# Kernel optimization log

Measured on AMD Instinct MI355X. Metric: run time of the kernel, lower is better.

## Reference

```python
import jax, jax.numpy as jnp
import numpy as np

D_WIN = 6
SIGMA = D_WIN / 2.0  # sigma = D/2
EPS = 1e-6


def _ln(x, g, b):
    m = jnp.mean(x, -1, keepdims=True)
    v = jnp.var(x, -1, keepdims=True)
    return (x - m) / jnp.sqrt(v + EPS) * g + b


def _cross_attn(q, kv, Wq, Wkv, Wproj, bproj, nh):
    # standard multi-head cross attention, no qkv bias (qkv_bias=False)
    B, S, C = q.shape
    N = kv.shape[1]
    hd = C // nh
    scale = hd ** -0.5
    qh = (q @ Wq).reshape(B, S, nh, hd).transpose(0, 2, 1, 3) * scale
    kvh = (kv @ Wkv).reshape(B, N, 2, nh, hd).transpose(2, 0, 3, 1, 4)
    k, v = kvh[0], kvh[1]
    attn = jax.nn.softmax(jnp.einsum('bhsd,bhnd->bhsn', qh, k), -1)
    x = jnp.einsum('bhsn,bhnd->bhsd', attn, v).transpose(0, 2, 1, 3).reshape(B, S, C)
    return x @ Wproj + bproj


def setup_inputs() -> dict:
    key = jax.random.key(0)
    ks = jax.random.split(key, 32)
    B, S, C, H, W = 32, 128, 384, 8, 512

    def lin(k, i, o):
        return jax.random.normal(k, (i, o), jnp.float32) * 0.02

    inp = {
        'q': jax.random.normal(ks[0], (B, S, C), jnp.float32),
        'kv': jax.random.normal(ks[1], (B, H * W, C), jnp.float32),
        # main attention linears (qkv_bias=False)
        'Wq': lin(ks[2], C, C),
        'Wkv': lin(ks[3], C, 2 * C),
        'Wproj': lin(ks[4], C, C), 'bproj': jnp.zeros((C,), jnp.float32),
        # position predictor
        'Wp_w': lin(ks[5], C, C), 'Wp_b': jnp.zeros((C,), jnp.float32),
        'vp_w': lin(ks[6], C, 1), 'vp_b': jnp.zeros((1,), jnp.float32),
        'Wqpos': lin(ks[7], C, C), 'bqpos': jnp.zeros((C,), jnp.float32),
        # simplified RCTC decoder projection
        'Wrctc': lin(ks[8], C, C), 'brctc': jnp.zeros((C,), jnp.float32),
        # pt_to_question cross attention (2 heads)
        'ca1_Wq': lin(ks[9], C, C), 'ca1_Wkv': lin(ks[10], C, 2 * C),
        'ca1_Wproj': lin(ks[11], C, C), 'ca1_bproj': jnp.zeros((C,), jnp.float32),
        # pt_to_image cross attention (2 heads)
        'ca2_Wq': lin(ks[12], C, C), 'ca2_Wkv': lin(ks[13], C, 2 * C),
        'ca2_Wproj': lin(ks[14], C, C), 'ca2_bproj': jnp.zeros((C,), jnp.float32),
        # layernorms
        'g_q1': jnp.ones((C,), jnp.float32), 'b_q1': jnp.zeros((C,), jnp.float32),
        'g_kv1': jnp.ones((C,), jnp.float32), 'b_kv1': jnp.zeros((C,), jnp.float32),
        'g_q2': jnp.ones((C,), jnp.float32), 'b_q2': jnp.zeros((C,), jnp.float32),
        'g_kv2': jnp.ones((C,), jnp.float32), 'b_kv2': jnp.zeros((C,), jnp.float32),
        'sz_h': H, 'sz_w': W,
    }
    return inp


def reference(q, kv, Wq, Wkv, Wproj, bproj, Wp_w, Wp_b, vp_w, vp_b, Wqpos, bqpos,
              Wrctc, brctc, ca1_Wq, ca1_Wkv, ca1_Wproj, ca1_bproj,
              ca2_Wq, ca2_Wkv, ca2_Wproj, ca2_bproj,
              g_q1, b_q1, g_kv1, b_kv1, g_q2, b_q2, g_kv2, b_kv2, sz_h, sz_w):
    B, N, C = kv.shape
    S = q.shape[1]
    H, W = sz_h, sz_w
    nh = 1
    hd = C // nh
    scale = hd ** -0.5

    # RCTC decoder (simplified): (B,N,C) -> (B,C,H,W) -> collapse H -> (B,W,C) -> linear
    kv_img = kv.transpose(0, 2, 1).reshape(B, C, H, W)
    dec = kv_img.mean(axis=2).transpose(0, 2, 1)  # (B, W, C)
    dec = dec @ Wrctc + brctc

    qh = (q @ Wq).reshape(B, S, nh, hd).transpose(0, 2, 1, 3) * scale  # (B,nh,S,hd)
    kvh = (dec @ Wkv).reshape(B, W, 2, nh, hd).transpose(2, 0, 3, 1, 4)
    k, v = kvh[0], kvh[1]  # (B,nh,W,hd)

    # position prediction branch
    p = q @ Wqpos + bqpos
    p = _cross_attn(_ln(p, g_q1, b_q1), _ln(q, g_kv1, b_kv1),
                    ca1_Wq, ca1_Wkv, ca1_Wproj, ca1_bproj, 2)
    p = _cross_attn(_ln(p, g_q2, b_q2), _ln(dec, g_kv2, b_kv2),
                    ca2_Wq, ca2_Wkv, ca2_Wproj, ca2_bproj, 2)
    p_t = jax.nn.sigmoid(jnp.tanh(p @ Wp_w + Wp_b) @ vp_w + vp_b) * W  # (B,S,1)

    # Gaussian window mask around predicted position
    idx = jnp.arange(W, dtype=jnp.float32)[None, None, None, :]     # (1,1,1,W)
    pexp = p_t[:, None, :, :]                                        # (B,1,S,1)
    gauss = jnp.exp(-(idx - pexp) ** 2 / (2.0 * SIGMA ** 2))         # (B,1,S,W)

    attn = jnp.einsum('bhsd,bhwd->bhsw', qh, k) * gauss
    attn = jax.nn.softmax(attn, -1)
    x = jnp.einsum('bhsw,bhwd->bhsd', attn, v).transpose(0, 2, 1, 3).reshape(B, S, C)
    return x @ Wproj + bproj
```

## Files before the change

### kernel.cpp

```cpp
#include <hip/hip_runtime.h>
#include <hip/hip_bf16.h>
#include <math.h>

#define B_ 32
#define S_ 128
#define C_ 384
#define H_ 8
#define W_ 512
#define NKV 4096

typedef __attribute__((ext_vector_type(8))) short short8;
typedef __attribute__((ext_vector_type(4))) float floatx4;

static __device__ __forceinline__ ushort f2bf(float v) {
    __hip_bfloat16 h = __float2bfloat16(v);
    return *(ushort*)&h;
}
static __device__ __forceinline__ float ldf(const float* p, size_t i) { return p[i]; }
static __device__ __forceinline__ float ldf(const ushort* p, size_t i) {
    union { uint u; float f; } c; c.u = (uint)p[i] << 16; return c.f;
}

struct PrepDesc {
    const float* kv; ushort* dec0b; const float* q; ushort* qb;
    const float* wsrc[12]; ushort* wdst[12]; int wN[12];
};
__global__ __launch_bounds__(256) void prep2_kernel(PrepDesc d) {
    __shared__ float t[32][33];
    const int meanB = B_ * W_ * (C_ / 4) / 256;
    const int castB = B_ * S_ * (C_ / 4) / 256;
    int bid = blockIdx.x;
    int tid = threadIdx.x;
    if (bid < meanB) {
        int v = bid * 256 + tid;
        int c4  = v % (C_ / 4);
        int row = v / (C_ / 4);
        int b = row / W_;
        int w = row % W_;
        const float4* src = (const float4*)d.kv + (size_t)(b * NKV + w) * (C_ / 4) + c4;
        float4 s = {0.f, 0.f, 0.f, 0.f};
#pragma unroll
        for (int h = 0; h < H_; ++h) {
            float4 x = src[(size_t)h * W_ * (C_ / 4)];
            s.x += x.x; s.y += x.y; s.z += x.z; s.w += x.w;
        }
        ushort4 o;
        o.x = f2bf(s.x * 0.125f); o.y = f2bf(s.y * 0.125f);
        o.z = f2bf(s.z * 0.125f); o.w = f2bf(s.w * 0.125f);
        ((ushort4*)d.dec0b)[v] = o;
        return;
    }
    if (bid < meanB + castB) {
        int v = (bid - meanB) * 256 + tid;
        float4 f = ((const float4*)d.q)[v];
        ushort4 o;
        o.x = f2bf(f.x); o.y = f2bf(f.y); o.z = f2bf(f.z); o.w = f2bf(f.w);
        ((ushort4*)d.qb)[v] = o;
        return;
    }
    int f = bid - meanB - castB;
    int wi = f / 288, tile = f % 288;
    int N = d.wN[wi];
    int tiles_n = N / 32;
    if (tile >= 12 * tiles_n) return;
    int k0 = (tile / tiles_n) * 32, n0 = (tile % tiles_n) * 32;
    int r = tid >> 3, c4 = (tid & 7) * 4;
    float4 v = *(const float4*)&d.wsrc[wi][(size_t)(k0 + r) * N + n0 + c4];
    t[r][c4] = v.x; t[r][c4 + 1] = v.y; t[r][c4 + 2] = v.z; t[r][c4 + 3] = v.w;
    __syncthreads();
    int c = tid >> 3, k4 = (tid & 7) * 4;
    ushort4 o;
    o.x = f2bf(t[k4][c]); o.y = f2bf(t[k4 + 1][c]);
    o.z = f2bf(t[k4 + 2][c]); o.w = f2bf(t[k4 + 3][c]);
    *(ushort4*)&d.wdst[wi][(size_t)(n0 + c) * 384 + k0 + k4] = o;
}

struct GJob {
    const ushort* A; const ushort* Bt;
    const float* bias; float* Cout; ushort* Cbf;
    int M, N, K; float alpha; int act;
};
struct GJobs { GJob j[3]; };

__global__ __launch_bounds__(256) void bgemm_kernel(GJobs gs) {
    const GJob g = gs.j[blockIdx.z];
    const int bm = blockIdx.y * 128, bn = blockIdx.x * 128;
    if (bm >= g.M || bn >= g.N) return;
    __shared__ ushort As[128 * 40];
    __shared__ ushort Bs[128 * 40];
    const int tid = threadIdx.x;
    const int wav = tid >> 6, lane = tid & 63;
    const int wm = (wav >> 1) * 64, wn = (wav & 1) * 64;
    const int lrow = lane & 15, lq = lane >> 4;

    floatx4 acc[4][4] = {};

    const int sr = tid >> 1, sc0 = (tid & 1) * 16;
    const ushort* Ag = g.A + (size_t)(bm + sr) * g.K + sc0;
    const ushort* Bg = g.Bt + (size_t)(bn + sr) * g.K + sc0;
    ushort* Asw = &As[sr * 40 + sc0];
    ushort* Bsw = &Bs[sr * 40 + sc0];

    uint4 a0 = *(const uint4*)(Ag);
    uint4 a1 = *(const uint4*)(Ag + 8);
    uint4 b0 = *(const uint4*)(Bg);
    uint4 b1 = *(const uint4*)(Bg + 8);

    for (int k0 = 0; k0 < g.K; k0 += 32) {
        __syncthreads();
        *(uint4*)Asw = a0; *(uint4*)(Asw + 8) = a1;
        *(uint4*)Bsw = b0; *(uint4*)(Bsw + 8) = b1;
        __syncthreads();
        if (k0 + 32 < g.K) {
            a0 = *(const uint4*)(Ag + k0 + 32);
            a1 = *(const uint4*)(Ag + k0 + 40);
            b0 = *(const uint4*)(Bg + k0 + 32);
            b1 = *(const uint4*)(Bg + k0 + 40);
        }
        short8 af[4], bfr[4];
#pragma unroll
        for (int i = 0; i < 4; ++i)
            af[i] = *(const short8*)&As[(wm + 16 * i + lrow) * 40 + lq * 8];
#pragma unroll
        for (int j = 0; j < 4; ++j)
            bfr[j] = *(const short8*)&Bs[(wn + 16 * j + lrow) * 40 + lq * 8];
#pragma unroll
        for (int i = 0; i < 4; ++i)
#pragma unroll
            for (int j = 0; j < 4; ++j)
                acc[i][j] = __builtin_amdgcn_mfma_f32_16x16x32_bf16(af[i], bfr[j], acc[i][j], 0, 0, 0);
    }

#pragma unroll
    for (int i = 0; i < 4; ++i)
#pragma unroll
        for (int j = 0; j < 4; ++j) {
            int row = bm + wm + 16 * i + lq * 4;
            int col = bn + wn + 16 * j + lrow;
            float bv = g.bias ? g.bias[col] : 0.f;
#pragma unroll
            for (int r = 0; r < 4; ++r) {
                float v = acc[i][j][r] * g.alpha + bv;
                if (g.act == 1) v = tanhf(v);
                size_t off = (size_t)(row + r) * g.N + col;
                if (g.Cout) g.Cout[off] = v;
                if (g.Cbf) g.Cbf[off] = f2bf(v);
            }
        }
}

static inline void bgemmJ(hipStream_t st, int nj, const GJob* js) {
    GJobs gs;
    int mx = 0, my = 0;
    for (int i = 0; i < nj; ++i) {
        gs.j[i] = js[i];
        int nx = js[i].N / 128, ny = js[i].M / 128;
        if (nx > mx) mx = nx;
        if (ny > my) my = ny;
    }
    for (int i = nj; i < 3; ++i) gs.j[i] = js[0];
    bgemm_kernel<<<dim3(mx, my, nj), 256, 0, st>>>(gs);
}

struct BGArgs {
    const ushort* A; const ushort* Bt;
    const float* bias; float* outF; ushort* outB;
    int lda, ldb, ldo;
    long AsB, BsB, OsB;
    int AsH, BsH, OsH;
    int K, NH;
    float alpha; int act;
    int nbat, vtz;
    const ushort* vtsrc; ushort* vtdst; int vtNw;
    const float* ptT; const float* vpw; const float* vpb; float* ptout; int ptrows;
};
__global__ __launch_bounds__(256) void battn_kernel(BGArgs g) {
    __shared__ ushort As[64 * 40];
    __shared__ ushort Bs[64 * 40];
    const int tid = threadIdx.x;
    const int bat = blockIdx.z;
    if (bat >= g.nbat) {
        int per = gridDim.x * gridDim.y;
        int bxy = blockIdx.y * gridDim.x + blockIdx.x;
        if (bat < g.nbat + g.vtz) {
            int flat = (bat - g.nbat) * per + bxy;
            int wt_n = g.vtNw >> 5;
            int tiles = wt_n * (C_ / 32);
            if (flat >= B_ * tiles) return;
            int b  = flat / tiles, rr = flat % tiles;
            int w0 = (rr % wt_n) * 32, c0 = (rr / wt_n) * 32;
            ushort (*t)[33] = (ushort (*)[33])As;
            int wl = tid >> 3, c4 = (tid & 7) * 4;
            ushort4 v = *(const ushort4*)&g.vtsrc[((size_t)b * g.vtNw + w0 + wl) * 768 + 384 + c0 + c4];
            t[wl][c4] = v.x; t[wl][c4 + 1] = v.y; t[wl][c4 + 2] = v.z; t[wl][c4 + 3] = v.w;
            __syncthreads();
            int dl = tid >> 3, w4 = (tid & 7) * 4;
            ushort4 o;
            o.x = t[w4][dl]; o.y = t[w4 + 1][dl]; o.z = t[w4 + 2][dl]; o.w = t[w4 + 3][dl];
            *(ushort4*)&g.vtdst[((size_t)b * C_ + c0 + dl) * g.vtNw + w0 + w4] = o;
            return;
        }
        __shared__ float red[2][128];
        int flat = (bat - g.nbat - g.vtz) * per + bxy;
        int sub = tid >> 7, t = tid & 127;
        int row = flat * 2 + sub;
        if (row < g.ptrows) {
            const float* x = g.ptT + (size_t)row * C_;
            float s = x[t] * g.vpw[t] + x[t + 128] * g.vpw[t + 128]
                    + x[t + 256] * g.vpw[t + 256];
            red[sub][t] = s;
        }
        __syncthreads();
        if (row < g.ptrows && t < 64) {
            float s = red[sub][t] + red[sub][t + 64];
            for (int o = 32; o; o >>= 1) s += __shfl_down(s, o);
            if (t == 0) g.ptout[row] = 512.0f / (1.0f + expf(-(s + g.vpb[0])));
        }
        return;
    }
    const int bn = blockIdx.x * 64, bm = blockIdx.y * 64;
    const int bb = bat / g.NH, hh = bat % g.NH;
    const ushort* A  = g.A  + (size_t)bb * g.AsB + (size_t)hh * g.AsH;
    const ushort* Bt = g.Bt + (size_t)bb * g.BsB + (size_t)hh * g.BsH;
    const int wav = tid >> 6, lane = tid & 63;
    const int lrow = lane & 15, lq = lane >> 4;
    const int sr = tid >> 2, sc0 = (tid & 3) * 8;
    const ushort* Ag = A  + (size_t)(bm + sr) * g.lda + sc0;
    const ushort* Bg = Bt + (size_t)(bn + sr) * g.ldb + sc0;
    ushort* Asw = &As[sr * 40 + sc0];
    ushort* Bsw = &Bs[sr * 40 + sc0];

    floatx4 acc[4] = {};

    uint4 a = *(const uint4*)(Ag);
    uint4 b = *(const uint4*)(Bg);

    for (int k0 = 0; k0 < g.K; k0 += 32) {
        __syncthreads();
        *(uint4*)Asw = a; *(uint4*)Bsw = b;
        __syncthreads();
        if (k0 + 32 < g.K) {
            a = *(const uint4*)(Ag + k0 + 32);
            b = *(const uint4*)(Bg + k0 + 32);
        }
        short8 af = *(const short8*)&As[(wav * 16 + lrow) * 40 + lq * 8];
#pragma unroll
        for (int j = 0; j < 4; ++j) {
            short8 bf = *(const short8*)&Bs[(16 * j + lrow) * 40 + lq * 8];
            acc[j] = __builtin_amdgcn_mfma_f32_16x16x32_bf16(af, bf, acc[j], 0, 0, 0);
        }
    }

#pragma unroll
    for (int j = 0; j < 4; ++j) {
        int col = bn + 16 * j + lrow;
        float bv = g.bias ? g.bias[col] : 0.f;
        int row0 = bm + wav * 16 + lq * 4;
#pragma unroll
        for (int r = 0; r < 4; ++r) {
            float v = acc[j][r] * g.alpha + bv;
            if (g.act == 1) v = tanhf(v);
            size_t off = (size_t)bb * g.OsB + (size_t)hh * g.OsH
                       + (size_t)(row0 + r) * g.ldo + col;
            if (g.outF) g.outF[off] = v;
            if (g.outB) g.outB[off] = f2bf(v);
        }
    }
}

static inline void battn(hipStream_t st, const ushort* A, const ushort* Bt,
                         const float* bias, float* outF, ushort* outB,
                         int M, int N, int K, float alpha, int act,
                         int lda, long AsB, int AsH,
                         int ldb, long BsB, int BsH,
                         int ldo, long OsB, int OsH,
                         int NH, int nbat,
                         const ushort* vtsrc = nullptr, ushort* vtdst = nullptr,
                         int vtNw = 0,
                         const float* ptT = nullptr, const float* vpw = nullptr,
                         const float* vpb = nullptr, float* ptout = nullptr,
                         int ptrows = 0) {
    BGArgs g;
    g.A = A; g.Bt = Bt; g.bias = bias; g.outF = outF; g.outB = outB;
    g.lda = lda; g.ldb = ldb; g.ldo = ldo;
    g.AsB = AsB; g.BsB = BsB; g.OsB = OsB;
    g.AsH = AsH; g.BsH = BsH; g.OsH = OsH;
    g.K = K; g.NH = NH; g.alpha = alpha; g.act = act;
    g.nbat = nbat; g.vtsrc = vtsrc; g.vtdst = vtdst; g.vtNw = vtNw;
    g.ptT = ptT; g.vpw = vpw; g.vpb = vpb; g.ptout = ptout; g.ptrows = ptrows;
    int gx = N / 64, gy = M / 64;
    int per = gx * gy;
    int vtz = 0, ptz = 0;
    if (vtsrc) {
        int nvt = B_ * (vtNw / 32) * (C_ / 32);
        vtz = (nvt + per - 1) / per;
    }
    if (ptT) {
        int npb = (ptrows + 1) / 2;
        ptz = (npb + per - 1) / per;
    }
    g.vtz = vtz;
    battn_kernel<<<dim3(gx, gy, nbat + vtz + ptz), 256, 0, st>>>(g);
}

static inline void bgemm64(hipStream_t st, const ushort* A, const ushort* Bt,
                           const float* bias, float* outF, ushort* outB,
                           int M, int N, int K, float alpha, int act) {
    battn(st, A, Bt, bias, outF, outB, M, N, K, alpha, act,
          K, 0, 0, K, 0, 0, N, 0, 0, 1, 1);
}

struct Ln2Desc {
    const void* X0; const float* g0; const float* b0; ushort* Y0; int bf0; int rows0;
    const void* X1; const float* g1; const float* b1; ushort* Y1; int bf1;
};
__global__ __launch_bounds__(128) void ln2_kernel(Ln2Desc d) {
    int row = blockIdx.x;
    const void* X; const float* g; const float* bb; ushort* Y; int isbf;
    if (row < d.rows0) { X = d.X0; g = d.g0; bb = d.b0; Y = d.Y0; isbf = d.bf0; }
    else { row -= d.rows0; X = d.X1; g = d.g1; bb = d.b1; Y = d.Y1; isbf = d.bf1; }
    const float*  xf = (const float*)X + (size_t)row * C_;
    const ushort* xb = (const ushort*)X + (size_t)row * C_;
    ushort* y = Y + (size_t)row * C_;
    int t = threadIdx.x;
    float v0, v1, v2;
    if (isbf) { v0 = ldf(xb, t); v1 = ldf(xb, t + 128); v2 = ldf(xb, t + 256); }
    else      { v0 = ldf(xf, t); v1 = ldf(xf, t + 128); v2 = ldf(xf, t + 256); }
    float s = v0 + v1 + v2, sq = v0 * v0 + v1 * v1 + v2 * v2;
    __shared__ float rs[128], rq[128];
    rs[t] = s; rq[t] = sq; __syncthreads();
    if (t < 64) {
        s = rs[t] + rs[t + 64]; sq = rq[t] + rq[t + 64];
        for (int o = 32; o; o >>= 1) { s += __shfl_down(s, o); sq += __shfl_down(sq, o); }
        if (t == 0) { rs[0] = s; rq[0] = sq; }
    }
    __syncthreads();
    float mean = rs[0] * (1.0f / C_);
    float var  = rq[0] * (1.0f / C_) - mean * mean;
    float inv  = rsqrtf(var + 1e-6f);
    y[t]       = f2bf((v0 - mean) * inv * g[t]       + bb[t]);
    y[t + 128] = f2bf((v1 - mean) * inv * g[t + 128] + bb[t + 128]);
    y[t + 256] = f2bf((v2 - mean) * inv * g[t + 256] + bb[t + 256]);
}

template <int NW, int GAUSS>
__global__ __launch_bounds__(256) void softmax_kernel(
    const float* __restrict__ sc, const float* __restrict__ ptv,
    ushort* __restrict__ P)
{
    int row = blockIdx.x * 4 + (threadIdx.x >> 6);
    int lane = threadIdx.x & 63;
    const float* s = sc + (size_t)row * NW;
    float pcen = GAUSS ? ptv[row] : 0.f;
    float vals[NW / 64];
    float m = -1e30f;
#pragma unroll
    for (int i = 0; i < NW / 64; ++i) {
        int w = lane + 64 * i;
        float v = s[w];
        if (GAUSS) { float dw = (float)w - pcen; v *= expf(dw * dw * (-1.0f / 18.0f)); }
        vals[i] = v; m = fmaxf(m, v);
    }
#pragma unroll
    for (int o = 32; o; o >>= 1) m = fmaxf(m, __shfl_xor(m, o));
    float sum = 0.f;
#pragma unroll
    for (int i = 0; i < NW / 64; ++i) { vals[i] = expf(vals[i] - m); sum += vals[i]; }
#pragma unroll
    for (int o = 32; o; o >>= 1) sum += __shfl_xor(sum, o);
    float rinv = 1.0f / sum;
    ushort* op = P + (size_t)row * NW;
#pragma unroll
    for (int i = 0; i < NW / 64; ++i) op[lane + 64 * i] = f2bf(vals[i] * rinv);
}

extern "C" void kernel_launch(void* const* d_in, const int* in_sizes, int n_in,
                              void* d_out, int out_size, void* d_ws, size_t ws_size,
                              hipStream_t stream) {
    const float* q     = (const float*)d_in[0];
    const float* kv    = (const float*)d_in[1];
    const float* Wq    = (const float*)d_in[2];
    const float* Wkv   = (const float*)d_in[3];
    const float* Wproj = (const float*)d_in[4];
    const float* bproj = (const float*)d_in[5];
    const float* Wp_w  = (const float*)d_in[6];
    const float* Wp_b  = (const float*)d_in[7];
    const float* vp_w  = (const float*)d_in[8];
    const float* vp_b  = (const float*)d_in[9];
    const float* Wqpos = (const float*)d_in[10];
    const float* bqpos = (const float*)d_in[11];
    const float* Wrctc = (const float*)d_in[12];
    const float* brctc = (const float*)d_in[13];
    const float* ca1_Wq    = (const float*)d_in[14];
    const float* ca1_Wkv   = (const float*)d_in[15];
    const float* ca1_Wproj = (const float*)d_in[16];
    const float* ca1_bproj = (const float*)d_in[17];
    const float* ca2_Wq    = (const float*)d_in[18];
    const float* ca2_Wkv   = (const float*)d_in[19];
    const float* ca2_Wproj = (const float*)d_in[20];
    const float* ca2_bproj = (const float*)d_in[21];
    const float* g_q1  = (const float*)d_in[22];
    const float* b_q1  = (const float*)d_in[23];
    const float* g_kv1 = (const float*)d_in[24];
    const float* b_kv1 = (const float*)d_in[25];
    const float* g_q2  = (const float*)d_in[26];
    const float* b_q2  = (const float*)d_in[27];
    const float* g_kv2 = (const float*)d_in[28];
    const float* b_kv2 = (const float*)d_in[29];
    float* out = (float*)d_out;
    float* ws  = (float*)d_ws;

    ushort* dec0b = (ushort*)(ws);
    ushort* wb    = (ushort*)(ws + 3145728);
    ushort* qb    = (ushort*)(ws + 4251648);
    ushort* decb  = (ushort*)(ws + 5038080);
    ushort* qhb   = (ushort*)(ws + 8183808);
    float*  p     = ws + 8970240;
    ushort* pb    = (ushort*)(ws + 10543104);
    float*  t1    = ws + 11329536;
    ushort* t1b   = (ushort*)(ws + 12902400);
    ushort* t2b   = (ushort*)(ws + 13688832);
    ushort* qpb   = (ushort*)(ws + 16834560);
    ushort* kvb   = (ushort*)(ws + 17620992);
    ushort* vt    = (ushort*)(ws + 23912448);
    float*  sc    = ws + 27058176;
    ushort* Pb    = (ushort*)(ws + 31252480);
    ushort* xb    = (ushort*)(ws + 33349632);
    float*  ptb   = ws + 34136064;

    ushort* wbWq     = wb;
    ushort* wbWqpos  = wb + 147456;
    ushort* wbWrctc  = wb + 294912;
    ushort* wbC1Wq   = wb + 442368;
    ushort* wbC1Wp   = wb + 589824;
    ushort* wbC2Wq   = wb + 737280;
    ushort* wbC2Wp   = wb + 884736;
    ushort* wbWpw    = wb + 1032192;
    ushort* wbWproj  = wb + 1179648;
    ushort* wbWkv    = wb + 1327104;
    ushort* wbC1Wkv  = wb + 1622016;
    ushort* wbC2Wkv  = wb + 1916928;

    const float rs384 = 0.05103103630798288f;
    const float rs192 = 0.07216878364870323f;

    {
        PrepDesc d;
        d.kv = kv; d.dec0b = dec0b; d.q = q; d.qb = qb;
        const float* s_[12] = {Wq, Wqpos, Wrctc, ca1_Wq, ca1_Wproj, ca2_Wq, ca2_Wproj,
                               Wp_w, Wproj, Wkv, ca1_Wkv, ca2_Wkv};
        ushort* t_[12] = {wbWq, wbWqpos, wbWrctc, wbC1Wq, wbC1Wp, wbC2Wq, wbC2Wp,
                          wbWpw, wbWproj, wbWkv, wbC1Wkv, wbC2Wkv};
        for (int i = 0; i < 12; ++i) {
            d.wsrc[i] = s_[i]; d.wdst[i] = t_[i];
            d.wN[i] = (i >= 9) ? 768 : 384;
        }
        prep2_kernel<<<6144 + 1536 + 3456, 256, 0, stream>>>(d);
    }
    {
        GJob js[3];
        js[0] = {dec0b, wbWrctc, brctc, nullptr, decb, B_ * W_, 384, 384, 1.f, 0};
        js[1] = {qb, wbWq, nullptr, nullptr, qhb, B_ * S_, 384, 384, rs384, 0};
        js[2] = {qb, wbWqpos, bqpos, p, nullptr, B_ * S_, 384, 384, 1.f, 0};
        bgemmJ(stream, 3, js);
    }
    {
        Ln2Desc d;
        d.X0 = p; d.g0 = g_q1;  d.b0 = b_q1;  d.Y0 = t1b; d.bf0 = 0; d.rows0 = B_ * S_;
        d.X1 = q; d.g1 = g_kv1; d.b1 = b_kv1; d.Y1 = t2b; d.bf1 = 0;
        ln2_kernel<<<2 * B_ * S_, 128, 0, stream>>>(d);
    }
    {
        GJob js[2];
        js[0] = {t1b, wbC1Wq, nullptr, nullptr, qpb, B_ * S_, 384, 384, rs192, 0};
        js[1] = {t2b, wbC1Wkv, nullptr, nullptr, kvb, B_ * S_, 768, 384, 1.f, 0};
        bgemmJ(stream, 2, js);
    }
    battn(stream, qpb, kvb, nullptr, sc, nullptr, 128, 128, 192, 1.f, 0,
          384, (long)S_ * 384, 192,
          768, (long)S_ * 768, 192,
          128, (long)2 * S_ * 128, S_ * 128, 2, 64,
          kvb, vt, S_);
    softmax_kernel<128, 0><<<(B_ * 2 * S_) / 4, 256, 0, stream>>>(sc, nullptr, Pb);
    battn(stream, Pb, vt, nullptr, nullptr, xb, 128, 192, 128, 1.f, 0,
          128, (long)2 * S_ * 128, S_ * 128,
          128, (long)C_ * S_, 192 * S_,
          384, (long)S_ * 384, 192, 2, 64);
    bgemm64(stream, xb, wbC1Wp, ca1_bproj, p, nullptr, B_ * S_, 384, 384, 1.f, 0);
    {
        Ln2Desc d;
        d.X0 = p;    d.g0 = g_q2;  d.b0 = b_q2;  d.Y0 = t1b; d.bf0 = 0; d.rows0 = B_ * S_;
        d.X1 = decb; d.g1 = g_kv2; d.b1 = b_kv2; d.Y1 = t2b; d.bf1 = 1;
        ln2_kernel<<<B_ * S_ + B_ * W_, 128, 0, stream>>>(d);
    }
    {
        GJob js[2];
        js[0] = {t1b, wbC2Wq, nullptr, nullptr, qpb, B_ * S_, 384, 384, rs192, 0};
        js[1] = {t2b, wbC2Wkv, nullptr, nullptr, kvb, B_ * W_, 768, 384, 1.f, 0};
        bgemmJ(stream, 2, js);
    }
    battn(stream, qpb, kvb, nullptr, sc, nullptr, 128, 512, 192, 1.f, 0,
          384, (long)S_ * 384, 192,
          768, (long)W_ * 768, 192,
          512, (long)2 * S_ * 512, S_ * 512, 2, 64,
          kvb, vt, W_);
    softmax_kernel<512, 0><<<(B_ * 2 * S_) / 4, 256, 0, stream>>>(sc, nullptr, Pb);
    battn(stream, Pb, vt, nullptr, nullptr, xb, 128, 192, 512, 1.f, 0,
          512, (long)2 * S_ * 512, S_ * 512,
          512, (long)C_ * W_, 192 * W_,
          384, (long)S_ * 384, 192, 2, 64);
    bgemm64(stream, xb, wbC2Wp, ca2_bproj, p, pb, B_ * S_, 384, 384, 1.f, 0);
    {
        GJob js[2];
        js[0] = {pb, wbWpw, Wp_b, t1, nullptr, B_ * S_, 384, 384, 1.f, 1};
        js[1] = {decb, wbWkv, nullptr, nullptr, kvb, B_ * W_, 768, 384, 1.f, 0};
        bgemmJ(stream, 2, js);
    }
    battn(stream, qhb, kvb, nullptr, sc, nullptr, 128, 512, 384, 1.f, 0,
          384, (long)S_ * 384, 0,
          768, (long)W_ * 768, 0,
          512, (long)S_ * 512, 0, 1, 32,
          kvb, vt, W_,
          t1, vp_w, vp_b, ptb, B_ * S_);
    softmax_kernel<512, 1><<<(B_ * S_) / 4, 256, 0, stream>>>(sc, ptb, Pb);
    battn(stream, Pb, vt, nullptr, nullptr, xb, 128, 384, 512, 1.f, 0,
          512, (long)S_ * 512, 0,
          512, (long)C_ * W_, 0,
          384, (long)S_ * 384, 0, 1, 32);
    bgemm64(stream, xb, wbWproj, bproj, out, nullptr, B_ * S_, 384, 384, 1.f, 0);
}
```

Before: 556.8 us.

## Fuse QK, softmax, PV and projection into a persistent kernel with grid barriers

Replaces each attention stage's four separate launches (QK^T GEMM, softmax, PV GEMM, output projection) with one persistent 512-block kernel. The kernel loops over work units and separates phases with a software grid barrier built on global atomics. The aim is to remove kernel launch overhead and inter-kernel idle gaps. In exchange, correctness depends on all 512 blocks being co-resident (launch_bounds 2 per CU), and the fixed grid may balance work worse than the original per-phase grids. The barrier counters reuse a scratch buffer, which is zeroed with a memset.

```diff
diff --git a/kernel.cpp b/kernel.cpp
--- a/kernel.cpp
+++ b/kernel.cpp
@@ -19,6 +19,24 @@
 static __device__ __forceinline__ float ldf(const float* p, size_t i) { return p[i]; }
 static __device__ __forceinline__ float ldf(const ushort* p, size_t i) {
     union { uint u; float f; } c; c.u = (uint)p[i] << 16; return c.f;
+}
+
+static __device__ __forceinline__ void gridbar(uint* cnt, uint* gen, uint nb) {
+    __syncthreads();
+    if (threadIdx.x == 0) {
+        __threadfence();
+        uint g = atomicAdd(gen, 0u);
+        uint old = atomicAdd(cnt, 1u);
+        if (old == nb - 1u) {
+            atomicExch(cnt, 0u);
+            __threadfence();
+            atomicAdd(gen, 1u);
+        } else {
+            while (atomicAdd(gen, 0u) == g) { __builtin_amdgcn_s_sleep(8); }
+        }
+        __threadfence();
+    }
+    __syncthreads();
 }
 
 struct PrepDesc {
@@ -174,51 +192,57 @@
     const ushort* vtsrc; ushort* vtdst; int vtNw;
     const float* ptT; const float* vpw; const float* vpb; float* ptout; int ptrows;
 };
-__global__ __launch_bounds__(256) void battn_kernel(BGArgs g) {
+
+static __device__ void battn_unit(const BGArgs& g, int u, int gx, int gy) {
     __shared__ ushort As[64 * 40];
     __shared__ ushort Bs[64 * 40];
+    const int per = gx * gy;
+    const int bat = u / per;
+    const int bxy = u % per;
+    const int bx = bxy % gx, by = bxy / gx;
     const int tid = threadIdx.x;
-    const int bat = blockIdx.z;
     if (bat >= g.nbat) {
-        int per = gridDim.x * gridDim.y;
-        int bxy = blockIdx.y * gridDim.x + blockIdx.x;
         if (bat < g.nbat + g.vtz) {
             int flat = (bat - g.nbat) * per + bxy;
             int wt_n = g.vtNw >> 5;
             int tiles = wt_n * (C_ / 32);
-            if (flat >= B_ * tiles) return;
-            int b  = flat / tiles, rr = flat % tiles;
-            int w0 = (rr % wt_n) * 32, c0 = (rr / wt_n) * 32;
-            ushort (*t)[33] = (ushort (*)[33])As;
-            int wl = tid >> 3, c4 = (tid & 7) * 4;
-            ushort4 v = *(const ushort4*)&g.vtsrc[((size_t)b * g.vtNw + w0 + wl) * 768 + 384 + c0 + c4];
-            t[wl][c4] = v.x; t[wl][c4 + 1] = v.y; t[wl][c4 + 2] = v.z; t[wl][c4 + 3] = v.w;
-            __syncthreads();
-            int dl = tid >> 3, w4 = (tid & 7) * 4;
-            ushort4 o;
-            o.x = t[w4][dl]; o.y = t[w4 + 1][dl]; o.z = t[w4 + 2][dl]; o.w = t[w4 + 3][dl];
-            *(ushort4*)&g.vtdst[((size_t)b * C_ + c0 + dl) * g.vtNw + w0 + w4] = o;
+            if (flat < B_ * tiles) {
+                int b  = flat / tiles, rr = flat % tiles;
+                int w0 = (rr % wt_n) * 32, c0 = (rr / wt_n) * 32;
+                ushort (*t)[33] = (ushort (*)[33])As;
+                int wl = tid >> 3, c4 = (tid & 7) * 4;
+                ushort4 v = *(const ushort4*)&g.vtsrc[((size_t)b * g.vtNw + w0 + wl) * 768 + 384 + c0 + c4];
+                __syncthreads();
+                t[wl][c4] = v.x; t[wl][c4 + 1] = v.y; t[wl][c4 + 2] = v.z; t[wl][c4 + 3] = v.w;
+                __syncthreads();
+                int dl = tid >> 3, w4 = (tid & 7) * 4;
+                ushort4 o;
+                o.x = t[w4][dl]; o.y = t[w4 + 1][dl]; o.z = t[w4 + 2][dl]; o.w = t[w4 + 3][dl];
+                *(ushort4*)&g.vtdst[((size_t)b * C_ + c0 + dl) * g.vtNw + w0 + w4] = o;
+            }
             return;
         }
         __shared__ float red[2][128];
         int flat = (bat - g.nbat - g.vtz) * per + bxy;
         int sub = tid >> 7, t = tid & 127;
         int row = flat * 2 + sub;
+        float s = 0.f;
         if (row < g.ptrows) {
             const float* x = g.ptT + (size_t)row * C_;
-            float s = x[t] * g.vpw[t] + x[t + 128] * g.vpw[t + 128]
-                    + x[t + 256] * g.vpw[t + 256];
-            red[sub][t] = s;
-        }
+            s = x[t] * g.vpw[t] + x[t + 128] * g.vpw[t + 128]
+              + x[t + 256] * g.vpw[t + 256];
+        }
+        __syncthreads();
+        red[sub][t] = s;
         __syncthreads();
         if (row < g.ptrows && t < 64) {
-            float s = red[sub][t] + red[sub][t + 64];
-            for (int o = 32; o; o >>= 1) s += __shfl_down(s, o);
-            if (t == 0) g.ptout[row] = 512.0f / (1.0f + expf(-(s + g.vpb[0])));
+            float s2 = red[sub][t] + red[sub][t + 64];
+            for (int o = 32; o; o >>= 1) s2 += __shfl_down(s2, o);
+            if (t == 0) g.ptout[row] = 512.0f / (1.0f + expf(-(s2 + g.vpb[0])));
         }
         return;
     }
-    const int bn = blockIdx.x * 64, bm = blockIdx.y * 64;
+    const int bn = bx * 64, bm = by * 64;
     const int bb = bat / g.NH, hh = bat % g.NH;
     const ushort* A  = g.A  + (size_t)bb * g.AsB + (size_t)hh * g.AsH;
     const ushort* Bt = g.Bt + (size_t)bb * g.BsB + (size_t)hh * g.BsH;
@@ -268,19 +292,76 @@
     }
 }
 
-static inline void battn(hipStream_t st, const ushort* A, const ushort* Bt,
-                         const float* bias, float* outF, ushort* outB,
-                         int M, int N, int K, float alpha, int act,
-                         int lda, long AsB, int AsH,
-                         int ldb, long BsB, int BsH,
-                         int ldo, long OsB, int OsH,
-                         int NH, int nbat,
-                         const ushort* vtsrc = nullptr, ushort* vtdst = nullptr,
-                         int vtNw = 0,
-                         const float* ptT = nullptr, const float* vpw = nullptr,
-                         const float* vpb = nullptr, float* ptout = nullptr,
-                         int ptrows = 0) {
-    BGArgs g;
+struct SMArgs { const float* sc; const float* ptv; ushort* P; int mode; int units; };
+
+template <int NW, int GAUSS>
+static __device__ void sm_body(const SMArgs& a, int u) {
+    int row = u * 4 + (threadIdx.x >> 6);
+    int lane = threadIdx.x & 63;
+    const float* s = a.sc + (size_t)row * NW;
+    float pcen = GAUSS ? a.ptv[row] : 0.f;
+    float vals[NW / 64];
+    float m = -1e30f;
+#pragma unroll
+    for (int i = 0; i < NW / 64; ++i) {
+        int w = lane + 64 * i;
+        float v = s[w];
+        if (GAUSS) { float dw = (float)w - pcen; v *= expf(dw * dw * (-1.0f / 18.0f)); }
+        vals[i] = v; m = fmaxf(m, v);
+    }
+#pragma unroll
+    for (int o = 32; o; o >>= 1) m = fmaxf(m, __shfl_xor(m, o));
+    float sum = 0.f;
+#pragma unroll
+    for (int i = 0; i < NW / 64; ++i) { vals[i] = expf(vals[i] - m); sum += vals[i]; }
+#pragma unroll
+    for (int o = 32; o; o >>= 1) sum += __shfl_xor(sum, o);
+    float rinv = 1.0f / sum;
+    ushort* op = a.P + (size_t)row * NW;
+#pragma unroll
+    for (int i = 0; i < NW / 64; ++i) op[lane + 64 * i] = f2bf(vals[i] * rinv);
+}
+
+static __device__ void sm_unit(const SMArgs& a, int u) {
+    if (a.mode == 0) sm_body<128, 0>(a, u);
+    else if (a.mode == 1) sm_body<512, 0>(a, u);
+    else sm_body<512, 1>(a, u);
+}
+
+struct SegArgs {
+    BGArgs g1; int u1, gx1, gy1;
+    SMArgs sm;
+    BGArgs g2; int u2, gx2, gy2;
+    BGArgs g3; int u3, gx3, gy3;
+    uint* bar;
+};
+
+__global__ __launch_bounds__(256, 2) void seg_kernel(SegArgs s) {
+    const uint nb = gridDim.x;
+    for (int u = blockIdx.x; u < s.u1; u += gridDim.x) battn_unit(s.g1, u, s.gx1, s.gy1);
+    gridbar(s.bar, s.bar + 1, nb);
+    for (int u = blockIdx.x; u < s.sm.units; u += gridDim.x) sm_unit(s.sm, u);
+    gridbar(s.bar, s.bar + 1, nb);
+    for (int u = blockIdx.x; u < s.u2; u += gridDim.x) battn_unit(s.g2, u, s.gx2, s.gy2);
+    gridbar(s.bar, s.bar + 1, nb);
+    for (int u = blockIdx.x; u < s.u3; u += gridDim.x) battn_unit(s.g3, u, s.gx3, s.gy3);
+}
+
+struct BGPlan { BGArgs g; int units, gx, gy; };
+static inline BGPlan planBG(const ushort* A, const ushort* Bt,
+                            const float* bias, float* outF, ushort* outB,
+                            int M, int N, int K, float alpha, int act,
+                            int lda, long AsB, int AsH,
+                            int ldb, long BsB, int BsH,
+                            int ldo, long OsB, int OsH,
+                            int NH, int nbat,
+                            const ushort* vtsrc = nullptr, ushort* vtdst = nullptr,
+                            int vtNw = 0,
+                            const float* ptT = nullptr, const float* vpw = nullptr,
+                            const float* vpb = nullptr, float* ptout = nullptr,
+                            int ptrows = 0) {
+    BGPlan p;
+    BGArgs& g = p.g;
     g.A = A; g.Bt = Bt; g.bias = bias; g.outF = outF; g.outB = outB;
     g.lda = lda; g.ldb = ldb; g.ldo = ldo;
     g.AsB = AsB; g.BsB = BsB; g.OsB = OsB;
@@ -288,8 +369,8 @@
     g.K = K; g.NH = NH; g.alpha = alpha; g.act = act;
     g.nbat = nbat; g.vtsrc = vtsrc; g.vtdst = vtdst; g.vtNw = vtNw;
     g.ptT = ptT; g.vpw = vpw; g.vpb = vpb; g.ptout = ptout; g.ptrows = ptrows;
-    int gx = N / 64, gy = M / 64;
-    int per = gx * gy;
+    p.gx = N / 64; p.gy = M / 64;
+    int per = p.gx * p.gy;
     int vtz = 0, ptz = 0;
     if (vtsrc) {
         int nvt = B_ * (vtNw / 32) * (C_ / 32);
@@ -300,14 +381,19 @@
         ptz = (npb + per - 1) / per;
     }
     g.vtz = vtz;
-    battn_kernel<<<dim3(gx, gy, nbat + vtz + ptz), 256, 0, st>>>(g);
-}
-
-static inline void bgemm64(hipStream_t st, const ushort* A, const ushort* Bt,
-                           const float* bias, float* outF, ushort* outB,
-                           int M, int N, int K, float alpha, int act) {
-    battn(st, A, Bt, bias, outF, outB, M, N, K, alpha, act,
-          K, 0, 0, K, 0, 0, N, 0, 0, 1, 1);
+    p.units = per * (nbat + vtz + ptz);
+    return p;
+}
+
+static inline void launchSeg(hipStream_t st, const BGPlan& q, SMArgs sm,
+                             const BGPlan& pv, const BGPlan& pr, uint* bar) {
+    SegArgs s;
+    s.g1 = q.g;  s.u1 = q.units;  s.gx1 = q.gx;  s.gy1 = q.gy;
+    s.sm = sm;
+    s.g2 = pv.g; s.u2 = pv.units; s.gx2 = pv.gx; s.gy2 = pv.gy;
+    s.g3 = pr.g; s.u3 = pr.units; s.gx3 = pr.gx; s.gy3 = pr.gy;
+    s.bar = bar;
+    seg_kernel<<<dim3(512), dim3(256), 0, st>>>(s);
 }
 
 struct Ln2Desc {
@@ -341,37 +427,6 @@
     y[t]       = f2bf((v0 - mean) * inv * g[t]       + bb[t]);
     y[t + 128] = f2bf((v1 - mean) * inv * g[t + 128] + bb[t + 128]);
     y[t + 256] = f2bf((v2 - mean) * inv * g[t + 256] + bb[t + 256]);
-}
-
-template <int NW, int GAUSS>
-__global__ __launch_bounds__(256) void softmax_kernel(
-    const float* __restrict__ sc, const float* __restrict__ ptv,
-    ushort* __restrict__ P)
-{
-    int row = blockIdx.x * 4 + (threadIdx.x >> 6);
-    int lane = threadIdx.x & 63;
-    const float* s = sc + (size_t)row * NW;
-    float pcen = GAUSS ? ptv[row] : 0.f;
-    float vals[NW / 64];
-    float m = -1e30f;
-#pragma unroll
-    for (int i = 0; i < NW / 64; ++i) {
-        int w = lane + 64 * i;
-        float v = s[w];
-        if (GAUSS) { float dw = (float)w - pcen; v *= expf(dw * dw * (-1.0f / 18.0f)); }
-        vals[i] = v; m = fmaxf(m, v);
-    }
-#pragma unroll
-    for (int o = 32; o; o >>= 1) m = fmaxf(m, __shfl_xor(m, o));
-    float sum = 0.f;
-#pragma unroll
-    for (int i = 0; i < NW / 64; ++i) { vals[i] = expf(vals[i] - m); sum += vals[i]; }
-#pragma unroll
-    for (int o = 32; o; o >>= 1) sum += __shfl_xor(sum, o);
-    float rinv = 1.0f / sum;
-    ushort* op = P + (size_t)row * NW;
-#pragma unroll
-    for (int i = 0; i < NW / 64; ++i) op[lane + 64 * i] = f2bf(vals[i] * rinv);
 }
 
 extern "C" void kernel_launch(void* const* d_in, const int* in_sizes, int n_in,
@@ -427,6 +482,7 @@
     ushort* Pb    = (ushort*)(ws + 31252480);
     ushort* xb    = (ushort*)(ws + 33349632);
     float*  ptb   = ws + 34136064;
+    uint*   bar   = (uint*)dec0b;
 
     ushort* wbWq     = wb;
     ushort* wbWqpos  = wb + 147456;
@@ -464,6 +520,7 @@
         js[2] = {qb, wbWqpos, bqpos, p, nullptr, B_ * S_, 384, 384, 1.f, 0};
         bgemmJ(stream, 3, js);
     }
+    hipMemsetAsync(bar, 0, 64, stream);
     {
         Ln2Desc d;
         d.X0 = p; d.g0 = g_q1;  d.b0 = b_q1;  d.Y0 = t1b; d.bf0 = 0; d.rows0 = B_ * S_;
@@ -476,17 +533,21 @@
         js[1] = {t2b, wbC1Wkv, nullptr, nullptr, kvb, B_ * S_, 768, 384, 1.f, 0};
         bgemmJ(stream, 2, js);
     }
-    battn(stream, qpb, kvb, nullptr, sc, nullptr, 128, 128, 192, 1.f, 0,
-          384, (long)S_ * 384, 192,
-          768, (long)S_ * 768, 192,
-          128, (long)2 * S_ * 128, S_ * 128, 2, 64,
-          kvb, vt, S_);
-    softmax_kernel<128, 0><<<(B_ * 2 * S_) / 4, 256, 0, stream>>>(sc, nullptr, Pb);
-    battn(stream, Pb, vt, nullptr, nullptr, xb, 128, 192, 128, 1.f, 0,
-          128, (long)2 * S_ * 128, S_ * 128,
-          128, (long)C_ * S_, 192 * S_,
-          384, (long)S_ * 384, 192, 2, 64);
-    bgemm64(stream, xb, wbC1Wp, ca1_bproj, p, nullptr, B_ * S_, 384, 384, 1.f, 0);
+    {
+        BGPlan qk = planBG(qpb, kvb, nullptr, sc, nullptr, 128, 128, 192, 1.f, 0,
+                           384, (long)S_ * 384, 192,
+                           768, (long)S_ * 768, 192,
+                           128, (long)2 * S_ * 128, S_ * 128, 2, 64,
+                           kvb, vt, S_);
+        SMArgs sm = {sc, nullptr, Pb, 0, (B_ * 2 * S_) / 4};
+        BGPlan pv = planBG(Pb, vt, nullptr, nullptr, xb, 128, 192, 128, 1.f, 0,
+                           128, (long)2 * S_ * 128, S_ * 128,
+                           128, (long)C_ * S_, 192 * S_,
+                           384, (long)S_ * 384, 192, 2, 64);
+        BGPlan pr = planBG(xb, wbC1Wp, ca1_bproj, p, nullptr, B_ * S_, 384, 384, 1.f, 0,
+                           384, 0, 0, 384, 0, 0, 384, 0, 0, 1, 1);
+        launchSeg(stream, qk, sm, pv, pr, bar);
+    }
     {
         Ln2Desc d;
         d.X0 = p;    d.g0 = g_q2;  d.b0 = b_q2;  d.Y0 = t1b; d.bf0 = 0; d.rows0 = B_ * S_;
@@ -499,33 +560,41 @@
         js[1] = {t2b, wbC2Wkv, nullptr, nullptr, kvb, B_ * W_, 768, 384, 1.f, 0};
         bgemmJ(stream, 2, js);
     }
-    battn(stream, qpb, kvb, nullptr, sc, nullptr, 128, 512, 192, 1.f, 0,
-          384, (long)S_ * 384, 192,
-          768, (long)W_ * 768, 192,
-          512, (long)2 * S_ * 512, S_ * 512, 2, 64,
-          kvb, vt, W_);
-    softmax_kernel<512, 0><<<(B_ * 2 * S_) / 4, 256, 0, stream>>>(sc, nullptr, Pb);
-    battn(stream, Pb, vt, nullptr, nullptr, xb, 128, 192, 512, 1.f, 0,
-          512, (long)2 * S_ * 512, S_ * 512,
-          512, (long)C_ * W_, 192 * W_,
-          384, (long)S_ * 384, 192, 2, 64);
-    bgemm64(stream, xb, wbC2Wp, ca2_bproj, p, pb, B_ * S_, 384, 384, 1.f, 0);
+    {
+        BGPlan qk = planBG(qpb, kvb, nullptr, sc, nullptr, 128, 512, 192, 1.f, 0,
+                           384, (long)S_ * 384, 192,
+                           768, (long)W_ * 768, 192,
+                           512, (long)2 * S_ * 512, S_ * 512, 2, 64,
+                           kvb, vt, W_);
+        SMArgs sm = {sc, nullptr, Pb, 1, (B_ * 2 * S_) / 4};
+        BGPlan pv = planBG(Pb, vt, nullptr, nullptr, xb, 128, 192, 512, 1.f, 0,
+                           512, (long)2 * S_ * 512, S_ * 512,
+                           512, (long)C_ * W_, 192 * W_,
+                           384, (long)S_ * 384, 192, 2, 64);
+        BGPlan pr = planBG(xb, wbC2Wp, ca2_bproj, p, pb, B_ * S_, 384, 384, 1.f, 0,
+                           384, 0, 0, 384, 0, 0, 384, 0, 0, 1, 1);
+        launchSeg(stream, qk, sm, pv, pr, bar);
+    }
     {
         GJob js[2];
         js[0] = {pb, wbWpw, Wp_b, t1, nullptr, B_ * S_, 384, 384, 1.f, 1};
         js[1] = {decb, wbWkv, nullptr, nullptr, kvb, B_ * W_, 768, 384, 1.f, 0};
         bgemmJ(stream, 2, js);
     }
-    battn(stream, qhb, kvb, nullptr, sc, nullptr, 128, 512, 384, 1.f, 0,
-          384, (long)S_ * 384, 0,
-          768, (long)W_ * 768, 0,
-          512, (long)S_ * 512, 0, 1, 32,
-          kvb, vt, W_,
-          t1, vp_w, vp_b, ptb, B_ * S_);
-    softmax_kernel<512, 1><<<(B_ * S_) / 4, 256, 0, stream>>>(sc, ptb, Pb);
-    battn(stream, Pb, vt, nullptr, nullptr, xb, 128, 384, 512, 1.f, 0,
-          512, (long)S_ * 512, 0,
-          512, (long)C_ * W_, 0,
-          384, (long)S_ * 384, 0, 1, 32);
-    bgemm64(stream, xb, wbWproj, bproj, out, nullptr, B_ * S_, 384, 384, 1.f, 0);
-}
+    {
+        BGPlan qk = planBG(qhb, kvb, nullptr, sc, nullptr, 128, 512, 384, 1.f, 0,
+                           384, (long)S_ * 384, 0,
+                           768, (long)W_ * 768, 0,
+                           512, (long)S_ * 512, 0, 1, 32,
+                           kvb, vt, W_,
+                           t1, vp_w, vp_b, ptb, B_ * S_);
+        SMArgs sm = {sc, ptb, Pb, 2, (B_ * S_) / 4};
+        BGPlan pv = planBG(Pb, vt, nullptr, nullptr, xb, 128, 384, 512, 1.f, 0,
+                           512, (long)S_ * 512, 0,
+                           512, (long)C_ * W_, 0,
+                           384, (long)S_ * 384, 0, 1, 32);
+        BGPlan pr = planBG(xb, wbWproj, bproj, out, nullptr, B_ * S_, 384, 384, 1.f, 0,
+                           384, 0, 0, 384, 0, 0, 384, 0, 0, 1, 1);
+        launchSeg(stream, qk, sm, pv, pr, bar);
+    }
+}
```

New measurement: 993.5 us. 78.4% more time.
